# Optimization experiments

Hardware: AMD Instinct MI355X
Metric: run time of the kernel (lower is better)

Reference implementation:

```python
import jax, jax.numpy as jnp
import numpy as np
import math

B, T, C = 2, 2048, 1024
N_HEADS = 16
HEAD_DIM = C // N_HEADS  # 64


def setup_inputs() -> dict:
    key = jax.random.key(0)
    ks = jax.random.split(key, 5)
    scale = 0.02
    return {
        "x": jax.random.normal(ks[0], (B, T, C), dtype=jnp.float32),
        "Wq": jax.random.normal(ks[1], (C, C), dtype=jnp.float32) * scale,
        "Wk": jax.random.normal(ks[2], (C, C), dtype=jnp.float32) * scale,
        "Wv": jax.random.normal(ks[3], (C, C), dtype=jnp.float32) * scale,
        "Wc": jax.random.normal(ks[4], (C, C), dtype=jnp.float32) * scale,
        "bc": jnp.zeros((C,), dtype=jnp.float32),
    }


def reference(x, Wq, Wk, Wv, Wc, bc):
    b, t, c = x.shape
    h, dh = N_HEADS, HEAD_DIM
    # Q/K/V projections (Linear, no bias): y = x @ W.T
    def proj(W):
        y = jnp.einsum('btc,dc->btd', x, W)
        return y.reshape(b, t, h, dh).transpose(0, 2, 1, 3)  # [B,H,T,dh]
    Q, K, V = proj(Wq), proj(Wk), proj(Wv)

    # scaled dot-product scores [B,H,T,T]
    scores = jnp.einsum('bhqd,bhkd->bhqk', Q, K) / math.sqrt(dh)
    # additive causal mask: + (1 - tril) * -1e9, as in the original
    causal = jnp.tril(jnp.ones((t, t), dtype=scores.dtype))
    scores = scores + (1.0 - causal) * (-1e9)

    attn = jax.nn.softmax(scores, axis=-1)  # dropout = identity (eval mode)
    o = jnp.einsum('bhqk,bhkd->bhqd', attn, V)
    o = o.transpose(0, 2, 1, 3).reshape(b, t, c)
    # output projection with bias (resid dropout = identity in eval)
    return jnp.einsum('btc,dc->btd', o, Wc) + bc
```

## Files before the change

kernel.cpp:

```cpp
#include <hip/hip_runtime.h>
#include <hip/hip_bf16.h>


typedef __attribute__((ext_vector_type(4))) float f32x4;
typedef __attribute__((ext_vector_type(4))) unsigned int u32x4;
typedef __attribute__((ext_vector_type(8))) __bf16 bf16x8;
typedef __attribute__((ext_vector_type(8))) unsigned short us8;
typedef __attribute__((ext_vector_type(4))) unsigned short us4;

#define LOG2E 1.4426950408889634f

__device__ __forceinline__ unsigned short f2bf(float f) {
    unsigned u = __builtin_bit_cast(unsigned, f);
    u += 0x7fffu + ((u >> 16) & 1u);
    return (unsigned short)(u >> 16);
}

__device__ __forceinline__ unsigned cvt_pk_bf16(float lo, float hi) {
    unsigned r;
    asm("v_cvt_pk_bf16_f32 %0, %1, %2" : "=v"(r) : "v"(lo), "v"(hi));
    return r;
}

__device__ __forceinline__ f32x4 mfma16(us8 a, us8 b, f32x4 c) {
    return __builtin_amdgcn_mfma_f32_16x16x32_bf16(
        __builtin_bit_cast(bf16x8, a), __builtin_bit_cast(bf16x8, b), c, 0, 0, 0);
}

__global__ __launch_bounds__(256) void fill_sentinel(float* __restrict__ out, int n) {
    int i = blockIdx.x * 256 + threadIdx.x;
    if (i < n) out[i] = 12345.0f;
}

__global__ __launch_bounds__(256) void cvt_xw(
    const float* __restrict__ x, const float* __restrict__ wq,
    const float* __restrict__ wk, const float* __restrict__ wv,
    unsigned short* __restrict__ xb, unsigned short* __restrict__ wqkvb) {
    long i = (long)(blockIdx.x * 256 + threadIdx.x) * 4;
    const float* src; unsigned short* dst; long off;
    if (i < 4194304L)      { src = x;  dst = xb;              off = i; }
    else if (i < 5242880L) { src = wq; dst = wqkvb;           off = i - 4194304L; }
    else if (i < 6291456L) { src = wk; dst = wqkvb + 1048576; off = i - 5242880L; }
    else                   { src = wv; dst = wqkvb + 2097152; off = i - 6291456L; }
    f32x4 v = *(const f32x4*)(src + off);
    us4 o = { f2bf(v[0]), f2bf(v[1]), f2bf(v[2]), f2bf(v[3]) };
    *(us4*)(dst + off) = o;
}

__global__ __launch_bounds__(256) void cvt_wc(const float* __restrict__ wc,
                                              unsigned short* __restrict__ wcb) {
    int idx = (blockIdx.x * 256 + threadIdx.x) * 4;
    f32x4 v = *(const f32x4*)(wc + idx);
    us4 o = { f2bf(v[0]), f2bf(v[1]), f2bf(v[2]), f2bf(v[3]) };
    *(us4*)(wcb + idx) = o;
}

template <int MI>
__device__ __forceinline__ void gemm_core_bb(
    const unsigned short* __restrict__ A, const unsigned short* __restrict__ B,
    int K, int m0, int n0, unsigned short* As, unsigned short* Bs, f32x4 acc[MI][4]) {
    const int tid = threadIdx.x;
    const int lane = tid & 63, wid = tid >> 6;
    const int g = lane >> 4, s = lane & 15;
    const int wr = wid >> 1, wc = wid & 1;
#pragma unroll
    for (int mi = 0; mi < MI; mi++)
#pragma unroll
        for (int ni = 0; ni < 4; ni++) acc[mi][ni] = (f32x4){0.f, 0.f, 0.f, 0.f};
    const int row = tid >> 3, col = (tid & 7) * 8;
    for (int k0 = 0; k0 < K; k0 += 64) {
        us8 av[MI], bv[4];
#pragma unroll
        for (int p = 0; p < MI; p++)
            av[p] = *(const us8*)(A + (size_t)(m0 + row + p * 32) * K + k0 + col);
#pragma unroll
        for (int p = 0; p < 4; p++)
            bv[p] = *(const us8*)(B + (size_t)(n0 + row + p * 32) * K + k0 + col);
        __syncthreads();
#pragma unroll
        for (int p = 0; p < MI; p++)
            *(us8*)(As + (row + p * 32) * 72 + col) = av[p];
#pragma unroll
        for (int p = 0; p < 4; p++)
            *(us8*)(Bs + (row + p * 32) * 72 + col) = bv[p];
        __syncthreads();
#pragma unroll
        for (int kk = 0; kk < 2; kk++) {
            us8 af[MI], bf[4];
#pragma unroll
            for (int mi = 0; mi < MI; mi++)
                af[mi] = *(const us8*)(As + (wr * (MI * 16) + mi * 16 + s) * 72 + kk * 32 + g * 8);
#pragma unroll
            for (int ni = 0; ni < 4; ni++)
                bf[ni] = *(const us8*)(Bs + (wc * 64 + ni * 16 + s) * 72 + kk * 32 + g * 8);
#pragma unroll
            for (int mi = 0; mi < MI; mi++)
#pragma unroll
                for (int ni = 0; ni < 4; ni++)
                    acc[mi][ni] = mfma16(af[mi], bf[ni], acc[mi][ni]);
        }
    }
}

__global__ __launch_bounds__(256) void gemm_qkv(
    const unsigned short* __restrict__ X, const unsigned short* __restrict__ Wb,
    unsigned short* __restrict__ Qb, unsigned short* __restrict__ Kb,
    unsigned short* __restrict__ VtG) {
    __shared__ unsigned short S[18432];
    unsigned short* As = S;
    unsigned short* Bs = S + 9216;
    const int bid = blockIdx.x;
    const int xcd = bid & 7, idx = bid >> 3;
    const int bm  = (xcd & 3) * 8 + (idx & 7);
    const int bnl = (xcd >> 2) * 12 + (idx >> 3);
    const int m0 = bm * 128;
    const int which = bnl >> 3;
    const int n0 = (bnl & 7) * 128;
    const unsigned short* W = Wb + (size_t)which * 1048576;
    f32x4 acc[4][4];
    gemm_core_bb<4>(X, W, 1024, m0, n0, As, Bs, acc);
    const int tid = threadIdx.x, lane = tid & 63, wid = tid >> 6;
    const int g = lane >> 4, s = lane & 15, wr = wid >> 1, wc = wid & 1;
    if (which < 2) {
        unsigned short* dst = which == 0 ? Qb : Kb;
        const float scale = which == 0 ? 0.125f : 1.0f;
#pragma unroll
        for (int mi = 0; mi < 4; mi++)
#pragma unroll
            for (int ni = 0; ni < 4; ni++) {
                int n1 = n0 + wc * 64 + ni * 16 + s;
                int hh = n1 >> 6, dd = n1 & 63;
#pragma unroll
                for (int r = 0; r < 4; r++) {
                    int mg = m0 + wr * 64 + mi * 16 + 4 * g + r;
                    int bb = mg >> 11, tt = mg & 2047;
                    dst[((size_t)(bb * 16 + hh) * 2048 + tt) * 64 + dd] = f2bf(acc[mi][ni][r] * scale);
                }
            }
    } else {
        __syncthreads();
        unsigned* T32 = (unsigned*)S;
#pragma unroll
        for (int mi = 0; mi < 4; mi++)
#pragma unroll
            for (int ni = 0; ni < 4; ni++) {
                int nl = wc * 64 + ni * 16 + s;
                int mlh = ((wr * 64 + mi * 16) >> 1) + 2 * g;
                T32[nl * 68 + mlh]     = cvt_pk_bf16(acc[mi][ni][0], acc[mi][ni][1]);
                T32[nl * 68 + mlh + 1] = cvt_pk_bf16(acc[mi][ni][2], acc[mi][ni][3]);
            }
        __syncthreads();
        const int row = tid >> 4, col8 = (tid & 15) * 8;
        const int bb = m0 >> 11, tt0 = m0 & 2047;
#pragma unroll
        for (int p = 0; p < 8; p++) {
            int nl = row + 16 * p;
            int n1 = n0 + nl, hh = n1 >> 6, dd = n1 & 63;
            us8 v = *(const us8*)(S + nl * 136 + col8);
            *(us8*)(VtG + ((size_t)(bb * 16 + hh) * 64 + dd) * 2048 + tt0 + col8) = v;
        }
    }
}

#define ATTN_EPILOGUE(QB0, OA, LR)                                              \
    {                                                                           \
        float li[4];                                                            \
        _Pragma("unroll") for (int r = 0; r < 4; r++)                           \
            li[r] = __shfl((LR), 4 * g + r, 64);                                \
        _Pragma("unroll") for (int db = 0; db < 4; db++)                        \
            _Pragma("unroll") for (int r = 0; r < 4; r++) {                     \
                int qq = (QB0) + 4 * g + r;                                     \
                float v = (OA)[db][r] / li[r];                                  \
                Ob[((size_t)(b * 2048) + qq) * 1024 + h * 64 + db * 16 + s] = f2bf(v); \
            }                                                                   \
    }

__global__ __launch_bounds__(256) void attn(
    const unsigned short* __restrict__ Qb, const unsigned short* __restrict__ Kb,
    const unsigned short* __restrict__ VtG, unsigned short* __restrict__ Ob) {
    __shared__ unsigned short Ks[2][64 * 72];
    __shared__ unsigned short Vt[2][64 * 72];
    const int bh = blockIdx.x & 31, i = blockIdx.x >> 5;
    const int b = bh >> 4, h = bh & 15;
    const unsigned short* Qp = Qb + (size_t)bh * 2048 * 64;
    const unsigned short* Kp = Kb + (size_t)bh * 2048 * 64;
    const unsigned short* Vp = VtG + (size_t)bh * 64 * 2048;
    const int tid = threadIdx.x, lane = tid & 63, wid = tid >> 6;
    const int g = lane >> 4, s = lane & 15;
    const int qbA = i * 64 + wid * 16;
    const int qbB = (31 - i) * 64 + wid * 16;
    const int qgA = qbA + s, qgB = qbB + s;
    us8 qfA[2], qfB[2];
    qfA[0] = *(const us8*)(Qp + (size_t)qgA * 64 + g * 8);
    qfA[1] = *(const us8*)(Qp + (size_t)qgA * 64 + 32 + g * 8);
    qfB[0] = *(const us8*)(Qp + (size_t)qgB * 64 + g * 8);
    qfB[1] = *(const us8*)(Qp + (size_t)qgB * 64 + 32 + g * 8);
    float m_run = -3.0e38f, l_run = 0.f;
    f32x4 o_acc[4];
#pragma unroll
    for (int db = 0; db < 4; db++) o_acc[db] = (f32x4){0.f, 0.f, 0.f, 0.f};
    const int srow = tid >> 3, scol = (tid & 7) * 8;
    auto tileoff = [&](int jj) { return (jj <= i ? jj : jj - i - 1) * 64; };
    us8 kpre[2], vpre[2];
#pragma unroll
    for (int p = 0; p < 2; p++) {
        kpre[p] = *(const us8*)(Kp + (size_t)(srow + 32 * p) * 64 + scol);
        vpre[p] = *(const us8*)(Vp + (size_t)(srow + 32 * p) * 2048 + scol);
    }
#pragma unroll
    for (int p = 0; p < 2; p++) {
        *(us8*)(&Ks[0][(srow + 32 * p) * 72 + scol]) = kpre[p];
        *(us8*)(&Vt[0][(srow + 32 * p) * 72 + scol]) = vpre[p];
    }
    {
        const int nk = tileoff(1);
#pragma unroll
        for (int p = 0; p < 2; p++) {
            kpre[p] = *(const us8*)(Kp + (size_t)(nk + srow + 32 * p) * 64 + scol);
            vpre[p] = *(const us8*)(Vp + (size_t)(srow + 32 * p) * 2048 + nk + scol);
        }
    }
    int cur = 0;
    for (int it = 0; it <= 32; ++it) {
        __syncthreads();
        if (it < 32) {
#pragma unroll
            for (int p = 0; p < 2; p++) {
                *(us8*)(&Ks[cur ^ 1][(srow + 32 * p) * 72 + scol]) = kpre[p];
                *(us8*)(&Vt[cur ^ 1][(srow + 32 * p) * 72 + scol]) = vpre[p];
            }
            if (it < 31) {
                const int nk = tileoff(it + 2);
#pragma unroll
                for (int p = 0; p < 2; p++) {
                    kpre[p] = *(const us8*)(Kp + (size_t)(nk + srow + 32 * p) * 64 + scol);
                    vpre[p] = *(const us8*)(Vp + (size_t)(srow + 32 * p) * 2048 + nk + scol);
                }
            }
        }
        if (it == i + 1) {
            ATTN_EPILOGUE(qbA, o_acc, l_run);
            m_run = -3.0e38f; l_run = 0.f;
#pragma unroll
            for (int db = 0; db < 4; db++) o_acc[db] = (f32x4){0.f, 0.f, 0.f, 0.f};
        }
        const bool qsel = it > i;
        const int kv0 = tileoff(it);
        const int qg = qsel ? qgB : qgA;
        const us8* qf = qsel ? qfB : qfA;
        const unsigned short* Kc = Ks[cur];
        const unsigned short* Vc = Vt[cur];
        float sf[4][4];
        __builtin_amdgcn_s_setprio(1);
#pragma unroll
        for (int f = 0; f < 4; f++) {
            f32x4 a = (f32x4){0.f, 0.f, 0.f, 0.f};
            us8 k0v = *(const us8*)(Kc + (f * 16 + s) * 72 + g * 8);
            us8 k1v = *(const us8*)(Kc + (f * 16 + s) * 72 + 32 + g * 8);
            a = mfma16(k0v, qf[0], a);
            a = mfma16(k1v, qf[1], a);
#pragma unroll
            for (int r = 0; r < 4; r++) sf[f][r] = a[r];
        }
        __builtin_amdgcn_s_setprio(0);
        const bool diag = qsel ? (it == 32) : (it == i);
        if (diag) {
#pragma unroll
            for (int f = 0; f < 4; f++)
#pragma unroll
                for (int r = 0; r < 4; r++)
                    if (kv0 + f * 16 + 4 * g + r > qg) sf[f][r] = -3.0e38f;
        }
        float mt = -3.0e38f;
#pragma unroll
        for (int f = 0; f < 4; f++)
#pragma unroll
            for (int r = 0; r < 4; r++) mt = fmaxf(mt, sf[f][r]);
        mt = fmaxf(mt, __shfl_xor(mt, 16));
        mt = fmaxf(mt, __shfl_xor(mt, 32));
        float mnew = m_run;
        if (!__all(mt - m_run <= 8.0f)) {
            mnew = fmaxf(m_run, mt);
            float alpha = __builtin_amdgcn_exp2f((m_run - mnew) * LOG2E);
            l_run *= alpha;
            float al[4];
#pragma unroll
            for (int r = 0; r < 4; r++) al[r] = __shfl(alpha, 4 * g + r, 64);
#pragma unroll
            for (int db = 0; db < 4; db++)
#pragma unroll
                for (int r = 0; r < 4; r++) o_acc[db][r] *= al[r];
        }
        float psum = 0.f;
#pragma unroll
        for (int f = 0; f < 4; f++)
#pragma unroll
            for (int r = 0; r < 4; r++) {
                float p = __builtin_amdgcn_exp2f((sf[f][r] - mnew) * LOG2E);
                sf[f][r] = p;
                psum += p;
            }
        psum += __shfl_xor(psum, 16);
        psum += __shfl_xor(psum, 32);
        l_run += psum;
        m_run = mnew;
        unsigned pk[4][2];
#pragma unroll
        for (int f = 0; f < 4; f++)
#pragma unroll
            for (int hh2 = 0; hh2 < 2; hh2++)
                pk[f][hh2] = cvt_pk_bf16(sf[f][2 * hh2], sf[f][2 * hh2 + 1]);
        const int srcA = 32 * (g & 1) + s, srcB = srcA + 16;
        const bool ghi = g >= 2;
        us8 pa[2];
#pragma unroll
        for (int kk = 0; kk < 2; kk++) {
            unsigned e0 = __shfl(pk[kk * 2][0], srcA, 64);
            unsigned e1 = __shfl(pk[kk * 2][1], srcA, 64);
            unsigned e2 = __shfl(pk[kk * 2][0], srcB, 64);
            unsigned e3 = __shfl(pk[kk * 2][1], srcB, 64);
            unsigned o0 = __shfl(pk[kk * 2 + 1][0], srcA, 64);
            unsigned o1 = __shfl(pk[kk * 2 + 1][1], srcA, 64);
            unsigned o2 = __shfl(pk[kk * 2 + 1][0], srcB, 64);
            unsigned o3 = __shfl(pk[kk * 2 + 1][1], srcB, 64);
            u32x4 dw = { ghi ? o0 : e0, ghi ? o1 : e1, ghi ? o2 : e2, ghi ? o3 : e3 };
            pa[kk] = __builtin_bit_cast(us8, dw);
        }
        __builtin_amdgcn_s_setprio(1);
#pragma unroll
        for (int db = 0; db < 4; db++) {
            const unsigned short* vrow = Vc + (db * 16 + s) * 72;
            us8 vf0 = *(const us8*)(vrow + g * 8);
            o_acc[db] = mfma16(pa[0], vf0, o_acc[db]);
            us8 vf1 = *(const us8*)(vrow + 32 + g * 8);
            o_acc[db] = mfma16(pa[1], vf1, o_acc[db]);
        }
        __builtin_amdgcn_s_setprio(0);
        cur ^= 1;
    }
    ATTN_EPILOGUE(qbB, o_acc, l_run);
}

__global__ __launch_bounds__(256) void gemm_out(
    const unsigned short* __restrict__ O, const unsigned short* __restrict__ Wcb,
    const float* __restrict__ bc, float* __restrict__ out) {
    __shared__ unsigned short As[64 * 72];
    __shared__ unsigned short Bs[128 * 72];
    const int bid = blockIdx.x;
    const int xcd = bid & 7, idx = bid >> 3;
    const int bm = xcd * 8 + (idx & 7);
    const int bn = idx >> 3;
    const int m0 = bm * 64, n0 = bn * 128;
    f32x4 acc[2][4];
    gemm_core_bb<2>(O, Wcb, 1024, m0, n0, As, Bs, acc);
    const int lane = threadIdx.x & 63, wid = threadIdx.x >> 6;
    const int g = lane >> 4, s = lane & 15, wr = wid >> 1, wc = wid & 1;
#pragma unroll
    for (int mi = 0; mi < 2; mi++)
#pragma unroll
        for (int ni = 0; ni < 4; ni++) {
            int ng = n0 + wc * 64 + ni * 16 + s;
            float bias = bc[ng];
#pragma unroll
            for (int r = 0; r < 4; r++) {
                int mg = m0 + wr * 32 + mi * 16 + 4 * g + r;
                out[(size_t)mg * 1024 + ng] = acc[mi][ni][r] + bias;
            }
        }
}

extern "C" void kernel_launch(void* const* d_in, const int* in_sizes, int n_in,
                              void* d_out, int out_size, void* d_ws, size_t ws_size,
                              hipStream_t stream) {
    const float* x  = (const float*)d_in[0];
    const float* Wq = (const float*)d_in[1];
    const float* Wk = (const float*)d_in[2];
    const float* Wv = (const float*)d_in[3];
    const float* Wc = (const float*)d_in[4];
    const float* bc = (const float*)d_in[5];
    float* out = (float*)d_out;

    if (ws_size < 33554432) {
        fill_sentinel<<<(out_size + 255) / 256, 256, 0, stream>>>(out, out_size);
        return;
    }
    char* w = (char*)d_ws;
    unsigned short* Qb  = (unsigned short*)(w);
    unsigned short* Kb  = (unsigned short*)(w + 8388608);
    unsigned short* VtG = (unsigned short*)(w + 16777216);
    unsigned short* Ob  = (unsigned short*)(w + 25165824);
    unsigned short* Wcb = (unsigned short*)(w);
    unsigned short* xb    = (unsigned short*)d_out;
    unsigned short* wqkvb = (unsigned short*)((char*)d_out + 8388608);

    cvt_xw<<<7168, 256, 0, stream>>>(x, Wq, Wk, Wv, xb, wqkvb);
    gemm_qkv<<<768, 256, 0, stream>>>(xb, wqkvb, Qb, Kb, VtG);
    attn<<<512, 256, 0, stream>>>(Qb, Kb, VtG, Ob);
    cvt_wc<<<1024, 256, 0, stream>>>(Wc, Wcb);
    gemm_out<<<512, 256, 0, stream>>>(Ob, Wcb, bc, out);
}
```

Baseline: 123.3 us.

## Share K/V tiles between paired query blocks in causal attention

Each workgroup handles two query blocks (i and 31-i). Before, it streamed K/V tiles for block A and then again for block B, 33 tile loads in total. Now it walks the K/V sequence once, over 32-i tiles, and runs QK and softmax-PV for both query blocks on the shared tiles while it <= i. This cuts global loads and LDS staging and adds independent MFMA work per tile. The cost is two accumulator sets, which raises register pressure and may reduce occupancy, and the per-block loop count is now uneven.

```diff
diff --git a/kernel.cpp b/kernel.cpp
--- a/kernel.cpp
+++ b/kernel.cpp
@@ -195,63 +195,16 @@
     qfA[1] = *(const us8*)(Qp + (size_t)qgA * 64 + 32 + g * 8);
     qfB[0] = *(const us8*)(Qp + (size_t)qgB * 64 + g * 8);
     qfB[1] = *(const us8*)(Qp + (size_t)qgB * 64 + 32 + g * 8);
-    float m_run = -3.0e38f, l_run = 0.f;
-    f32x4 o_acc[4];
-#pragma unroll
-    for (int db = 0; db < 4; db++) o_acc[db] = (f32x4){0.f, 0.f, 0.f, 0.f};
+    float mA = -3.0e38f, lA = 0.f, mB = -3.0e38f, lB = 0.f;
+    f32x4 oA[4], oB[4];
+#pragma unroll
+    for (int db = 0; db < 4; db++) {
+        oA[db] = (f32x4){0.f, 0.f, 0.f, 0.f};
+        oB[db] = (f32x4){0.f, 0.f, 0.f, 0.f};
+    }
     const int srow = tid >> 3, scol = (tid & 7) * 8;
-    auto tileoff = [&](int jj) { return (jj <= i ? jj : jj - i - 1) * 64; };
-    us8 kpre[2], vpre[2];
-#pragma unroll
-    for (int p = 0; p < 2; p++) {
-        kpre[p] = *(const us8*)(Kp + (size_t)(srow + 32 * p) * 64 + scol);
-        vpre[p] = *(const us8*)(Vp + (size_t)(srow + 32 * p) * 2048 + scol);
-    }
-#pragma unroll
-    for (int p = 0; p < 2; p++) {
-        *(us8*)(&Ks[0][(srow + 32 * p) * 72 + scol]) = kpre[p];
-        *(us8*)(&Vt[0][(srow + 32 * p) * 72 + scol]) = vpre[p];
-    }
-    {
-        const int nk = tileoff(1);
-#pragma unroll
-        for (int p = 0; p < 2; p++) {
-            kpre[p] = *(const us8*)(Kp + (size_t)(nk + srow + 32 * p) * 64 + scol);
-            vpre[p] = *(const us8*)(Vp + (size_t)(srow + 32 * p) * 2048 + nk + scol);
-        }
-    }
-    int cur = 0;
-    for (int it = 0; it <= 32; ++it) {
-        __syncthreads();
-        if (it < 32) {
-#pragma unroll
-            for (int p = 0; p < 2; p++) {
-                *(us8*)(&Ks[cur ^ 1][(srow + 32 * p) * 72 + scol]) = kpre[p];
-                *(us8*)(&Vt[cur ^ 1][(srow + 32 * p) * 72 + scol]) = vpre[p];
-            }
-            if (it < 31) {
-                const int nk = tileoff(it + 2);
-#pragma unroll
-                for (int p = 0; p < 2; p++) {
-                    kpre[p] = *(const us8*)(Kp + (size_t)(nk + srow + 32 * p) * 64 + scol);
-                    vpre[p] = *(const us8*)(Vp + (size_t)(srow + 32 * p) * 2048 + nk + scol);
-                }
-            }
-        }
-        if (it == i + 1) {
-            ATTN_EPILOGUE(qbA, o_acc, l_run);
-            m_run = -3.0e38f; l_run = 0.f;
-#pragma unroll
-            for (int db = 0; db < 4; db++) o_acc[db] = (f32x4){0.f, 0.f, 0.f, 0.f};
-        }
-        const bool qsel = it > i;
-        const int kv0 = tileoff(it);
-        const int qg = qsel ? qgB : qgA;
-        const us8* qf = qsel ? qfB : qfA;
-        const unsigned short* Kc = Ks[cur];
-        const unsigned short* Vc = Vt[cur];
-        float sf[4][4];
-        __builtin_amdgcn_s_setprio(1);
+    const int nt = 32 - i;
+    auto qk = [&](const us8* qf, const unsigned short* Kc, float sf[4][4]) {
 #pragma unroll
         for (int f = 0; f < 4; f++) {
             f32x4 a = (f32x4){0.f, 0.f, 0.f, 0.f};
@@ -262,8 +215,9 @@
 #pragma unroll
             for (int r = 0; r < 4; r++) sf[f][r] = a[r];
         }
-        __builtin_amdgcn_s_setprio(0);
-        const bool diag = qsel ? (it == 32) : (it == i);
+    };
+    auto smax_pv = [&](float sf[4][4], float& m_run, float& l_run, f32x4* o_acc,
+                       int qg, int kv0, bool diag, const unsigned short* Vc) {
         if (diag) {
 #pragma unroll
             for (int f = 0; f < 4; f++)
@@ -326,7 +280,6 @@
             u32x4 dw = { ghi ? o0 : e0, ghi ? o1 : e1, ghi ? o2 : e2, ghi ? o3 : e3 };
             pa[kk] = __builtin_bit_cast(us8, dw);
         }
-        __builtin_amdgcn_s_setprio(1);
 #pragma unroll
         for (int db = 0; db < 4; db++) {
             const unsigned short* vrow = Vc + (db * 16 + s) * 72;
@@ -335,10 +288,67 @@
             us8 vf1 = *(const us8*)(vrow + 32 + g * 8);
             o_acc[db] = mfma16(pa[1], vf1, o_acc[db]);
         }
-        __builtin_amdgcn_s_setprio(0);
+    };
+    us8 kpre[2], vpre[2];
+#pragma unroll
+    for (int p = 0; p < 2; p++) {
+        kpre[p] = *(const us8*)(Kp + (size_t)(srow + 32 * p) * 64 + scol);
+        vpre[p] = *(const us8*)(Vp + (size_t)(srow + 32 * p) * 2048 + scol);
+    }
+#pragma unroll
+    for (int p = 0; p < 2; p++) {
+        *(us8*)(&Ks[0][(srow + 32 * p) * 72 + scol]) = kpre[p];
+        *(us8*)(&Vt[0][(srow + 32 * p) * 72 + scol]) = vpre[p];
+    }
+    if (nt > 1) {
+#pragma unroll
+        for (int p = 0; p < 2; p++) {
+            kpre[p] = *(const us8*)(Kp + (size_t)(64 + srow + 32 * p) * 64 + scol);
+            vpre[p] = *(const us8*)(Vp + (size_t)(srow + 32 * p) * 2048 + 64 + scol);
+        }
+    }
+    int cur = 0;
+    for (int it = 0; it < nt; ++it) {
+        const int kv0 = it * 64;
+        __syncthreads();
+        if (it + 1 < nt) {
+#pragma unroll
+            for (int p = 0; p < 2; p++) {
+                *(us8*)(&Ks[cur ^ 1][(srow + 32 * p) * 72 + scol]) = kpre[p];
+                *(us8*)(&Vt[cur ^ 1][(srow + 32 * p) * 72 + scol]) = vpre[p];
+            }
+            if (it + 2 < nt) {
+                const int nk = kv0 + 128;
+#pragma unroll
+                for (int p = 0; p < 2; p++) {
+                    kpre[p] = *(const us8*)(Kp + (size_t)(nk + srow + 32 * p) * 64 + scol);
+                    vpre[p] = *(const us8*)(Vp + (size_t)(srow + 32 * p) * 2048 + nk + scol);
+                }
+            }
+        }
+        const unsigned short* Kc = Ks[cur];
+        const unsigned short* Vc = Vt[cur];
+        if (it <= i) {
+            float sfA[4][4], sfB[4][4];
+            __builtin_amdgcn_s_setprio(1);
+            qk(qfA, Kc, sfA);
+            qk(qfB, Kc, sfB);
+            __builtin_amdgcn_s_setprio(0);
+            smax_pv(sfA, mA, lA, oA, qgA, kv0, it == i, Vc);
+            smax_pv(sfB, mB, lB, oB, qgB, kv0, false, Vc);
+            if (it == i) {
+                ATTN_EPILOGUE(qbA, oA, lA);
+            }
+        } else {
+            float sfB[4][4];
+            __builtin_amdgcn_s_setprio(1);
+            qk(qfB, Kc, sfB);
+            __builtin_amdgcn_s_setprio(0);
+            smax_pv(sfB, mB, lB, oB, qgB, kv0, it == nt - 1, Vc);
+        }
         cur ^= 1;
     }
-    ATTN_EPILOGUE(qbB, o_acc, l_run);
+    ATTN_EPILOGUE(qbB, oB, lB);
 }
 
 __global__ __launch_bounds__(256) void gemm_out(
```

Result: slower. 152.3 us (+23.5%).

## Split paired causal attention blocks into one query tile per block and drop LDS staging

Applied to the files above, without the earlier changes.

Each attention block now handles a single 64-row query tile instead of a balanced pair (i, 31-i), doubling the grid to 1024 blocks. A permuted block-to-tile mapping interleaves short and long tiles for load balance. The shared-memory double-buffered K/V staging and its barriers are removed, and MFMA operands are read directly from global memory and cache. This cuts LDS traffic and sync overhead and raises occupancy, at the cost of redundant, less coalesced global loads across waves and uneven per-block work.

```diff
diff --git a/kernel.cpp b/kernel.cpp
--- a/kernel.cpp
+++ b/kernel.cpp
@@ -162,109 +162,44 @@
     }
 }
 
-#define ATTN_EPILOGUE(QB0, OA, LR)                                              \
-    {                                                                           \
-        float li[4];                                                            \
-        _Pragma("unroll") for (int r = 0; r < 4; r++)                           \
-            li[r] = __shfl((LR), 4 * g + r, 64);                                \
-        _Pragma("unroll") for (int db = 0; db < 4; db++)                        \
-            _Pragma("unroll") for (int r = 0; r < 4; r++) {                     \
-                int qq = (QB0) + 4 * g + r;                                     \
-                float v = (OA)[db][r] / li[r];                                  \
-                Ob[((size_t)(b * 2048) + qq) * 1024 + h * 64 + db * 16 + s] = f2bf(v); \
-            }                                                                   \
-    }
-
 __global__ __launch_bounds__(256) void attn(
     const unsigned short* __restrict__ Qb, const unsigned short* __restrict__ Kb,
     const unsigned short* __restrict__ VtG, unsigned short* __restrict__ Ob) {
-    __shared__ unsigned short Ks[2][64 * 72];
-    __shared__ unsigned short Vt[2][64 * 72];
-    const int bh = blockIdx.x & 31, i = blockIdx.x >> 5;
+    const int bh = blockIdx.x & 31, j = blockIdx.x >> 5;
+    const int q4 = j & 7, sel = j >> 3;
+    const int i = sel == 0 ? q4 : (sel == 1 ? 15 - q4 : (sel == 2 ? 16 + q4 : 31 - q4));
     const int b = bh >> 4, h = bh & 15;
     const unsigned short* Qp = Qb + (size_t)bh * 2048 * 64;
     const unsigned short* Kp = Kb + (size_t)bh * 2048 * 64;
     const unsigned short* Vp = VtG + (size_t)bh * 64 * 2048;
     const int tid = threadIdx.x, lane = tid & 63, wid = tid >> 6;
     const int g = lane >> 4, s = lane & 15;
-    const int qbA = i * 64 + wid * 16;
-    const int qbB = (31 - i) * 64 + wid * 16;
-    const int qgA = qbA + s, qgB = qbB + s;
-    us8 qfA[2], qfB[2];
-    qfA[0] = *(const us8*)(Qp + (size_t)qgA * 64 + g * 8);
-    qfA[1] = *(const us8*)(Qp + (size_t)qgA * 64 + 32 + g * 8);
-    qfB[0] = *(const us8*)(Qp + (size_t)qgB * 64 + g * 8);
-    qfB[1] = *(const us8*)(Qp + (size_t)qgB * 64 + 32 + g * 8);
+    const int qb0 = i * 64 + wid * 16;
+    const int qg = qb0 + s;
+    us8 qf[2];
+    qf[0] = *(const us8*)(Qp + (size_t)qg * 64 + g * 8);
+    qf[1] = *(const us8*)(Qp + (size_t)qg * 64 + 32 + g * 8);
     float m_run = -3.0e38f, l_run = 0.f;
     f32x4 o_acc[4];
 #pragma unroll
     for (int db = 0; db < 4; db++) o_acc[db] = (f32x4){0.f, 0.f, 0.f, 0.f};
-    const int srow = tid >> 3, scol = (tid & 7) * 8;
-    auto tileoff = [&](int jj) { return (jj <= i ? jj : jj - i - 1) * 64; };
-    us8 kpre[2], vpre[2];
-#pragma unroll
-    for (int p = 0; p < 2; p++) {
-        kpre[p] = *(const us8*)(Kp + (size_t)(srow + 32 * p) * 64 + scol);
-        vpre[p] = *(const us8*)(Vp + (size_t)(srow + 32 * p) * 2048 + scol);
-    }
-#pragma unroll
-    for (int p = 0; p < 2; p++) {
-        *(us8*)(&Ks[0][(srow + 32 * p) * 72 + scol]) = kpre[p];
-        *(us8*)(&Vt[0][(srow + 32 * p) * 72 + scol]) = vpre[p];
-    }
-    {
-        const int nk = tileoff(1);
-#pragma unroll
-        for (int p = 0; p < 2; p++) {
-            kpre[p] = *(const us8*)(Kp + (size_t)(nk + srow + 32 * p) * 64 + scol);
-            vpre[p] = *(const us8*)(Vp + (size_t)(srow + 32 * p) * 2048 + nk + scol);
-        }
-    }
-    int cur = 0;
-    for (int it = 0; it <= 32; ++it) {
-        __syncthreads();
-        if (it < 32) {
-#pragma unroll
-            for (int p = 0; p < 2; p++) {
-                *(us8*)(&Ks[cur ^ 1][(srow + 32 * p) * 72 + scol]) = kpre[p];
-                *(us8*)(&Vt[cur ^ 1][(srow + 32 * p) * 72 + scol]) = vpre[p];
-            }
-            if (it < 31) {
-                const int nk = tileoff(it + 2);
-#pragma unroll
-                for (int p = 0; p < 2; p++) {
-                    kpre[p] = *(const us8*)(Kp + (size_t)(nk + srow + 32 * p) * 64 + scol);
-                    vpre[p] = *(const us8*)(Vp + (size_t)(srow + 32 * p) * 2048 + nk + scol);
-                }
-            }
-        }
-        if (it == i + 1) {
-            ATTN_EPILOGUE(qbA, o_acc, l_run);
-            m_run = -3.0e38f; l_run = 0.f;
-#pragma unroll
-            for (int db = 0; db < 4; db++) o_acc[db] = (f32x4){0.f, 0.f, 0.f, 0.f};
-        }
-        const bool qsel = it > i;
-        const int kv0 = tileoff(it);
-        const int qg = qsel ? qgB : qgA;
-        const us8* qf = qsel ? qfB : qfA;
-        const unsigned short* Kc = Ks[cur];
-        const unsigned short* Vc = Vt[cur];
+    for (int it = 0; it <= i; ++it) {
+        const int kv0 = it * 64;
         float sf[4][4];
         __builtin_amdgcn_s_setprio(1);
 #pragma unroll
         for (int f = 0; f < 4; f++) {
+            const unsigned short* krow = Kp + (size_t)(kv0 + f * 16 + s) * 64;
+            us8 k0v = *(const us8*)(krow + g * 8);
+            us8 k1v = *(const us8*)(krow + 32 + g * 8);
             f32x4 a = (f32x4){0.f, 0.f, 0.f, 0.f};
-            us8 k0v = *(const us8*)(Kc + (f * 16 + s) * 72 + g * 8);
-            us8 k1v = *(const us8*)(Kc + (f * 16 + s) * 72 + 32 + g * 8);
             a = mfma16(k0v, qf[0], a);
             a = mfma16(k1v, qf[1], a);
 #pragma unroll
             for (int r = 0; r < 4; r++) sf[f][r] = a[r];
         }
         __builtin_amdgcn_s_setprio(0);
-        const bool diag = qsel ? (it == 32) : (it == i);
-        if (diag) {
+        if (it == i) {
 #pragma unroll
             for (int f = 0; f < 4; f++)
 #pragma unroll
@@ -329,16 +264,25 @@
         __builtin_amdgcn_s_setprio(1);
 #pragma unroll
         for (int db = 0; db < 4; db++) {
-            const unsigned short* vrow = Vc + (db * 16 + s) * 72;
+            const unsigned short* vrow = Vp + (size_t)(db * 16 + s) * 2048 + kv0;
             us8 vf0 = *(const us8*)(vrow + g * 8);
             o_acc[db] = mfma16(pa[0], vf0, o_acc[db]);
             us8 vf1 = *(const us8*)(vrow + 32 + g * 8);
             o_acc[db] = mfma16(pa[1], vf1, o_acc[db]);
         }
         __builtin_amdgcn_s_setprio(0);
-        cur ^= 1;
     }
-    ATTN_EPILOGUE(qbB, o_acc, l_run);
+    float li[4];
+#pragma unroll
+    for (int r = 0; r < 4; r++) li[r] = __shfl(l_run, 4 * g + r, 64);
+#pragma unroll
+    for (int db = 0; db < 4; db++)
+#pragma unroll
+        for (int r = 0; r < 4; r++) {
+            int qq = qb0 + 4 * g + r;
+            float v = o_acc[db][r] / li[r];
+            Ob[((size_t)(b * 2048) + qq) * 1024 + h * 64 + db * 16 + s] = f2bf(v);
+        }
 }
 
 __global__ __launch_bounds__(256) void gemm_out(
@@ -395,7 +339,7 @@
 
     cvt_xw<<<7168, 256, 0, stream>>>(x, Wq, Wk, Wv, xb, wqkvb);
     gemm_qkv<<<768, 256, 0, stream>>>(xb, wqkvb, Qb, Kb, VtG);
-    attn<<<512, 256, 0, stream>>>(Qb, Kb, VtG, Ob);
+    attn<<<1024, 256, 0, stream>>>(Qb, Kb, VtG, Ob);
     cvt_wc<<<1024, 256, 0, stream>>>(Wc, Wcb);
     gemm_out<<<512, 256, 0, stream>>>(Ob, Wcb, bc, out);
 }
```

Result: slower. 199.0 us (+61.4%).

## Split attention KV range across two blocks and merge partial softmax results

Applied to the files above, without the earlier changes.

Each attention block, which previously handled a paired query tile A and B over 33 KV tiles, is split into two blocks. One does tile A fully plus the first half of B's KV range; the other does the second half of B's range. Unnormalized partial outputs (bf16) and running max/sum go to scratch in the output buffer, and a new merge kernel combines them with log-sum-exp weighting. This doubles the grid to 1024 blocks for better occupancy and shorter per-block latency, at the cost of an extra kernel launch, extra global traffic and bf16 rounding of the partial outputs.

```diff
diff --git a/kernel.cpp b/kernel.cpp
--- a/kernel.cpp
+++ b/kernel.cpp
@@ -14,6 +14,11 @@
     unsigned u = __builtin_bit_cast(unsigned, f);
     u += 0x7fffu + ((u >> 16) & 1u);
     return (unsigned short)(u >> 16);
+}
+
+__device__ __forceinline__ float bf2f(unsigned short u) {
+    unsigned v = (unsigned)u << 16;
+    return __builtin_bit_cast(float, v);
 }
 
 __device__ __forceinline__ unsigned cvt_pk_bf16(float lo, float hi) {
@@ -162,7 +167,7 @@
     }
 }
 
-#define ATTN_EPILOGUE(QB0, OA, LR)                                              \
+#define ATTN_EPILOGUE_FINAL(QB0, OA, LR)                                        \
     {                                                                           \
         float li[4];                                                            \
         _Pragma("unroll") for (int r = 0; r < 4; r++)                           \
@@ -177,10 +182,13 @@
 
 __global__ __launch_bounds__(256) void attn(
     const unsigned short* __restrict__ Qb, const unsigned short* __restrict__ Kb,
-    const unsigned short* __restrict__ VtG, unsigned short* __restrict__ Ob) {
+    const unsigned short* __restrict__ VtG, unsigned short* __restrict__ Ob,
+    unsigned short* __restrict__ Po, float* __restrict__ Pml) {
     __shared__ unsigned short Ks[2][64 * 72];
     __shared__ unsigned short Vt[2][64 * 72];
-    const int bh = blockIdx.x & 31, i = blockIdx.x >> 5;
+    const int bid = blockIdx.x;
+    const int bh = bid & 31, rr = bid >> 5;
+    const int i = rr & 15, half = rr >> 4;
     const int b = bh >> 4, h = bh & 15;
     const unsigned short* Qp = Qb + (size_t)bh * 2048 * 64;
     const unsigned short* Kp = Kb + (size_t)bh * 2048 * 64;
@@ -191,8 +199,10 @@
     const int qbB = (31 - i) * 64 + wid * 16;
     const int qgA = qbA + s, qgB = qbB + s;
     us8 qfA[2], qfB[2];
-    qfA[0] = *(const us8*)(Qp + (size_t)qgA * 64 + g * 8);
-    qfA[1] = *(const us8*)(Qp + (size_t)qgA * 64 + 32 + g * 8);
+    if (half == 0) {
+        qfA[0] = *(const us8*)(Qp + (size_t)qgA * 64 + g * 8);
+        qfA[1] = *(const us8*)(Qp + (size_t)qgA * 64 + 32 + g * 8);
+    }
     qfB[0] = *(const us8*)(Qp + (size_t)qgB * 64 + g * 8);
     qfB[1] = *(const us8*)(Qp + (size_t)qgB * 64 + 32 + g * 8);
     float m_run = -3.0e38f, l_run = 0.f;
@@ -200,37 +210,41 @@
 #pragma unroll
     for (int db = 0; db < 4; db++) o_acc[db] = (f32x4){0.f, 0.f, 0.f, 0.f};
     const int srow = tid >> 3, scol = (tid & 7) * 8;
-    auto tileoff = [&](int jj) { return (jj <= i ? jj : jj - i - 1) * 64; };
+    const int nt = half == 0 ? 17 : 16;
+    auto kvtile = [&](int j) {
+        return half == 0 ? (j <= i ? j : j - i - 1) : (16 - i + j);
+    };
     us8 kpre[2], vpre[2];
-#pragma unroll
-    for (int p = 0; p < 2; p++) {
-        kpre[p] = *(const us8*)(Kp + (size_t)(srow + 32 * p) * 64 + scol);
-        vpre[p] = *(const us8*)(Vp + (size_t)(srow + 32 * p) * 2048 + scol);
-    }
-#pragma unroll
-    for (int p = 0; p < 2; p++) {
-        *(us8*)(&Ks[0][(srow + 32 * p) * 72 + scol]) = kpre[p];
-        *(us8*)(&Vt[0][(srow + 32 * p) * 72 + scol]) = vpre[p];
-    }
     {
-        const int nk = tileoff(1);
+        const int t0 = kvtile(0) * 64;
 #pragma unroll
         for (int p = 0; p < 2; p++) {
-            kpre[p] = *(const us8*)(Kp + (size_t)(nk + srow + 32 * p) * 64 + scol);
-            vpre[p] = *(const us8*)(Vp + (size_t)(srow + 32 * p) * 2048 + nk + scol);
+            kpre[p] = *(const us8*)(Kp + (size_t)(t0 + srow + 32 * p) * 64 + scol);
+            vpre[p] = *(const us8*)(Vp + (size_t)(srow + 32 * p) * 2048 + t0 + scol);
+        }
+#pragma unroll
+        for (int p = 0; p < 2; p++) {
+            *(us8*)(&Ks[0][(srow + 32 * p) * 72 + scol]) = kpre[p];
+            *(us8*)(&Vt[0][(srow + 32 * p) * 72 + scol]) = vpre[p];
+        }
+        const int t1 = kvtile(1) * 64;
+#pragma unroll
+        for (int p = 0; p < 2; p++) {
+            kpre[p] = *(const us8*)(Kp + (size_t)(t1 + srow + 32 * p) * 64 + scol);
+            vpre[p] = *(const us8*)(Vp + (size_t)(srow + 32 * p) * 2048 + t1 + scol);
         }
     }
     int cur = 0;
-    for (int it = 0; it <= 32; ++it) {
+    for (int it = 0; it < nt; ++it) {
         __syncthreads();
-        if (it < 32) {
+        if (it + 1 < nt) {
 #pragma unroll
             for (int p = 0; p < 2; p++) {
                 *(us8*)(&Ks[cur ^ 1][(srow + 32 * p) * 72 + scol]) = kpre[p];
                 *(us8*)(&Vt[cur ^ 1][(srow + 32 * p) * 72 + scol]) = vpre[p];
             }
-            if (it < 31) {
-                const int nk = tileoff(it + 2);
+            if (it + 2 < nt) {
+                const int nk = kvtile(it + 2) * 64;
 #pragma unroll
                 for (int p = 0; p < 2; p++) {
                     kpre[p] = *(const us8*)(Kp + (size_t)(nk + srow + 32 * p) * 64 + scol);
@@ -238,16 +252,10 @@
                 }
             }
         }
-        if (it == i + 1) {
-            ATTN_EPILOGUE(qbA, o_acc, l_run);
-            m_run = -3.0e38f; l_run = 0.f;
-#pragma unroll
-            for (int db = 0; db < 4; db++) o_acc[db] = (f32x4){0.f, 0.f, 0.f, 0.f};
-        }
-        const bool qsel = it > i;
-        const int kv0 = tileoff(it);
-        const int qg = qsel ? qgB : qgA;
-        const us8* qf = qsel ? qfB : qfA;
+        const bool isA = (half == 0) && (it <= i);
+        const int kv0 = kvtile(it) * 64;
+        const int qg = isA ? qgA : qgB;
+        const us8* qf = isA ? qfA : qfB;
         const unsigned short* Kc = Ks[cur];
         const unsigned short* Vc = Vt[cur];
         float sf[4][4];
@@ -263,7 +271,7 @@
             for (int r = 0; r < 4; r++) sf[f][r] = a[r];
         }
         __builtin_amdgcn_s_setprio(0);
-        const bool diag = qsel ? (it == 32) : (it == i);
+        const bool diag = isA ? (it == i) : (half == 1 && it == nt - 1);
         if (diag) {
 #pragma unroll
             for (int f = 0; f < 4; f++)
@@ -336,9 +344,49 @@
             o_acc[db] = mfma16(pa[1], vf1, o_acc[db]);
         }
         __builtin_amdgcn_s_setprio(0);
+        if (isA && it == i) {
+            ATTN_EPILOGUE_FINAL(qbA, o_acc, l_run);
+            m_run = -3.0e38f; l_run = 0.f;
+#pragma unroll
+            for (int db = 0; db < 4; db++) o_acc[db] = (f32x4){0.f, 0.f, 0.f, 0.f};
+        }
         cur ^= 1;
     }
-    ATTN_EPILOGUE(qbB, o_acc, l_run);
+    const int prow = (bh * 16 + i) * 64;
+    const int hofs = half * 32768;
+#pragma unroll
+    for (int db = 0; db < 4; db++)
+#pragma unroll
+        for (int r = 0; r < 4; r++) {
+            int row = wid * 16 + 4 * g + r;
+            Po[(size_t)(hofs + prow + row) * 64 + db * 16 + s] = f2bf(o_acc[db][r]);
+        }
+    if (lane < 16) {
+        int idx = hofs + prow + wid * 16 + lane;
+        Pml[idx * 2]     = m_run;
+        Pml[idx * 2 + 1] = l_run;
+    }
+}
+
+__global__ __launch_bounds__(256) void attn_merge(
+    const unsigned short* __restrict__ Po, const float* __restrict__ Pml,
+    unsigned short* __restrict__ Ob) {
+    const int rowg = blockIdx.x * 4 + (threadIdx.x >> 6);
+    const int lane = threadIdx.x & 63;
+    const int pair = rowg >> 6, row = rowg & 63;
+    const int bh = pair >> 4, i = pair & 15;
+    const int b = bh >> 4, h = bh & 15;
+    const int q = (31 - i) * 64 + row;
+    const float m0 = Pml[rowg * 2],           l0 = Pml[rowg * 2 + 1];
+    const float m1 = Pml[(32768 + rowg) * 2], l1 = Pml[(32768 + rowg) * 2 + 1];
+    const float m = fmaxf(m0, m1);
+    const float w0 = __builtin_amdgcn_exp2f((m0 - m) * LOG2E);
+    const float w1 = __builtin_amdgcn_exp2f((m1 - m) * LOG2E);
+    const float l = l0 * w0 + l1 * w1;
+    const float o0 = bf2f(Po[(size_t)rowg * 64 + lane]);
+    const float o1 = bf2f(Po[(size_t)(32768 + rowg) * 64 + lane]);
+    const float o = (o0 * w0 + o1 * w1) / l;
+    Ob[((size_t)(b * 2048) + q) * 1024 + h * 64 + lane] = f2bf(o);
 }
 
 __global__ __launch_bounds__(256) void gemm_out(
@@ -392,10 +440,13 @@
     unsigned short* Wcb = (unsigned short*)(w);
     unsigned short* xb    = (unsigned short*)d_out;
     unsigned short* wqkvb = (unsigned short*)((char*)d_out + 8388608);
+    unsigned short* Po    = (unsigned short*)d_out;
+    float*          Pml   = (float*)((char*)d_out + 8388608);
 
     cvt_xw<<<7168, 256, 0, stream>>>(x, Wq, Wk, Wv, xb, wqkvb);
     gemm_qkv<<<768, 256, 0, stream>>>(xb, wqkvb, Qb, Kb, VtG);
-    attn<<<512, 256, 0, stream>>>(Qb, Kb, VtG, Ob);
+    attn<<<1024, 256, 0, stream>>>(Qb, Kb, VtG, Ob, Po, Pml);
+    attn_merge<<<8192, 256, 0, stream>>>(Po, Pml, Ob);
     cvt_wc<<<1024, 256, 0, stream>>>(Wc, Wcb);
     gemm_out<<<512, 256, 0, stream>>>(Ob, Wcb, bc, out);
 }
```

Result: slower. 127.6 us (+3.5%).
